# Performance work log

Measured on AMD Instinct MI355X. Metric: run time of the kernel, lower is better.

## Reference

```python
import jax, jax.numpy as jnp
import numpy as np

IN_DIM, MEM_DIM, NUM_WORDS, N_LEAVES = 300, 256, 50000, 8192


def setup_inputs() -> dict:
    key = jax.random.key(0)
    ks = jax.random.split(key, 6)
    s = 0.05
    return {
        "embs": jax.random.normal(ks[0], (N_LEAVES, IN_DIM), jnp.float32),
        "Wx": jax.random.normal(ks[1], (4 * MEM_DIM, IN_DIM), jnp.float32) * s,
        "bx": jax.random.normal(ks[2], (4 * MEM_DIM,), jnp.float32) * s,
        "Wl": jax.random.normal(ks[3], (5 * MEM_DIM, MEM_DIM), jnp.float32) * s,
        "Wr": jax.random.normal(ks[4], (5 * MEM_DIM, MEM_DIM), jnp.float32) * s,
        "emb_table": jax.random.normal(ks[5], (NUM_WORDS, IN_DIM), jnp.float32),
    }


def reference(embs, Wx, bx, Wl, Wr, emb_table):
    m = Wl.shape[1]

    # x-projection order along fused axis: [cx, ix, fx, ox]
    def proj_x(x):  # [B, in] -> [B, 4, m]
        return (x @ Wx.T + bx).reshape(x.shape[0], 4, m)

    # hidden-projection order: [u, i, lf, rf, o]
    def compose(xg, lc, lh, rc, rh):
        lg = (lh @ Wl.T).reshape(-1, 5, m)
        rg = (rh @ Wr.T).reshape(-1, 5, m)
        u = jnp.tanh(xg[:, 0] + lg[:, 0] + rg[:, 0])
        i = jax.nn.sigmoid(xg[:, 1] + lg[:, 1] + rg[:, 1])
        lf = jax.nn.sigmoid(xg[:, 2] + lg[:, 2] + rg[:, 2])  # fx shared
        rf = jax.nn.sigmoid(xg[:, 2] + lg[:, 3] + rg[:, 3])  # fx shared
        c = i * u + lf * lc + rf * rc
        o = jax.nn.sigmoid(xg[:, 3] + lg[:, 4] + rg[:, 4])
        h = o * jnp.tanh(c)
        return c, h

    # leaves: zero child states, per-leaf embedding inputs
    L = embs.shape[0]
    z = jnp.zeros((L, m), embs.dtype)
    c, h = compose(proj_x(embs), z, z, z, z)

    # internal nodes (PAD=True): input is word_embedding(num_words - 1)
    pad_xg = proj_x(emb_table[-1:])  # [1, 4, m]

    while c.shape[0] > 1:  # static shapes; 13 merge levels
        lc, rc = c[0::2], c[1::2]
        lh, rh = h[0::2], h[1::2]
        B = lc.shape[0]
        c, h = compose(jnp.broadcast_to(pad_xg, (B, 4, m)), lc, lh, rc, rh)

    return jnp.stack([c, h])  # root (c, h): [2, 1, mem_dim]
```

## Files before the change

### kernel.cpp

```cpp
#include <hip/hip_runtime.h>
#include <math.h>


#define MEM 256

typedef __attribute__((ext_vector_type(8))) short bf16x8;
typedef __attribute__((ext_vector_type(4))) float f32x4;

__device__ __forceinline__ float sigf(float x) { return 1.0f / (1.0f + __expf(-x)); }

__device__ __forceinline__ unsigned short f2b(float f) {
  unsigned int u = __float_as_uint(f);
  u = (u + 0x7FFFu + ((u >> 16) & 1u)) >> 16;
  return (unsigned short)u;
}

#define NB_WCF 2560
#define NB_WXF 960
#define NB_EB 10240
__global__ __launch_bounds__(256) void k_prep(
    const float* __restrict__ Wl, const float* __restrict__ Wr,
    const float* __restrict__ Wx, const float* __restrict__ bx,
    const float* __restrict__ embs, const float* __restrict__ emb_last,
    unsigned short* __restrict__ Wcf, unsigned short* __restrict__ Wxf,
    unsigned short* __restrict__ eb, float* __restrict__ bias5) {
  int b = blockIdx.x;
  if (b < NB_WCF) {
    int idx = b * 256 + threadIdx.x;
    int f = idx >> 9, r = idx & 511;
    int lane = r >> 3, j = r & 7;
    int gate = f % 5, t = f / 5;
    int grp = t & 15, kc = t >> 4;
    int k = kc * 32 + ((lane >> 4) << 3) + j;
    int n = gate * 256 + (grp << 4) + (lane & 15);
    float v = (k < 256) ? Wl[n * 256 + k] : Wr[n * 256 + (k - 256)];
    Wcf[idx] = f2b(v);
  } else if (b < NB_WCF + NB_WXF) {
    int idx = (b - NB_WCF) * 256 + threadIdx.x;
    int f = idx >> 9, r = idx & 511;
    int lane = r >> 3, j = r & 7;
    int gate = f % 3, t = f / 3;
    int grp = t & 15, kc = t >> 4;
    int k = kc * 32 + ((lane >> 4) << 3) + j;
    const int gmap[3] = {0, 1, 3};
    int n = gmap[gate] * 256 + (grp << 4) + (lane & 15);
    float v = (k < 300) ? Wx[n * 300 + k] : 0.0f;
    Wxf[idx] = f2b(v);
  } else if (b < NB_WCF + NB_WXF + NB_EB) {
    int idx = (b - NB_WCF - NB_WXF) * 256 + threadIdx.x;
    int row = idx / 320;
    int k = idx - row * 320;
    eb[idx] = (k < 300) ? f2b(embs[row * 300 + k]) : (unsigned short)0;
  } else {
    int g = b - (NB_WCF + NB_WXF + NB_EB);
    __shared__ float er[300];
    for (int k = threadIdx.x; k < 300; k += 256) er[k] = emb_last[k];
    __syncthreads();
    const int map[5] = {0, 1, 2, 2, 3};
    int wrow = map[g] * 256 + threadIdx.x;
    const float* w = Wx + wrow * 300;
    float s = bx[wrow];
    for (int k = 0; k < 300; k++) s += er[k] * w[k];
    bias5[g * 256 + threadIdx.x] = s;
  }
}

__global__ __launch_bounds__(256) void k_leaf_mfma(
    const unsigned short* __restrict__ eb, const unsigned short* __restrict__ Wxf,
    const float* __restrict__ bx, float* __restrict__ cO,
    unsigned short* __restrict__ hO) {
  int lane = threadIdx.x & 63;
  int wave = threadIdx.x >> 6;
  int grp = blockIdx.y;
  int tb = (blockIdx.x * 4 + wave) * 2;
  int m = lane & 15, quad = lane >> 4;

  f32x4 acc[2][3];
#pragma unroll
  for (int rt = 0; rt < 2; rt++)
#pragma unroll
    for (int g = 0; g < 3; g++) acc[rt][g] = (f32x4){0.f, 0.f, 0.f, 0.f};

  const unsigned short* ar0 = eb + (tb * 16 + m) * 320 + quad * 8;
  const unsigned short* ar1 = eb + ((tb + 1) * 16 + m) * 320 + quad * 8;
#pragma unroll
  for (int kc = 0; kc < 10; kc++) {
    const unsigned short* bp = Wxf + ((kc * 16 + grp) * 3) * 512 + lane * 8;
    bf16x8 b0 = *(const bf16x8*)(bp);
    bf16x8 b1 = *(const bf16x8*)(bp + 512);
    bf16x8 b2 = *(const bf16x8*)(bp + 1024);
    bf16x8 a0 = *(const bf16x8*)(ar0 + kc * 32);
    bf16x8 a1 = *(const bf16x8*)(ar1 + kc * 32);
    acc[0][0] = __builtin_amdgcn_mfma_f32_16x16x32_bf16(a0, b0, acc[0][0], 0, 0, 0);
    acc[0][1] = __builtin_amdgcn_mfma_f32_16x16x32_bf16(a0, b1, acc[0][1], 0, 0, 0);
    acc[0][2] = __builtin_amdgcn_mfma_f32_16x16x32_bf16(a0, b2, acc[0][2], 0, 0, 0);
    acc[1][0] = __builtin_amdgcn_mfma_f32_16x16x32_bf16(a1, b0, acc[1][0], 0, 0, 0);
    acc[1][1] = __builtin_amdgcn_mfma_f32_16x16x32_bf16(a1, b1, acc[1][1], 0, 0, 0);
    acc[1][2] = __builtin_amdgcn_mfma_f32_16x16x32_bf16(a1, b2, acc[1][2], 0, 0, 0);
  }
  int col = grp * 16 + m;
  float b0 = bx[col], b1 = bx[256 + col], b3 = bx[768 + col];
#pragma unroll
  for (int rt = 0; rt < 2; rt++) {
#pragma unroll
    for (int reg = 0; reg < 4; reg++) {
      int row = (tb + rt) * 16 + quad * 4 + reg;
      float u = tanhf(acc[rt][0][reg] + b0);
      float ig = sigf(acc[rt][1][reg] + b1);
      float o = sigf(acc[rt][2][reg] + b3);
      float c = ig * u;
      cO[row * MEM + col] = c;
      hO[row * MEM + col] = f2b(o * tanhf(c));
    }
  }
}

template <int RT>
__global__ __launch_bounds__(256) void k_compose_mfma(
    const unsigned short* __restrict__ hprev,
    const float* __restrict__ cprev,
    const unsigned short* __restrict__ Wcf, const float* __restrict__ bias5,
    float* __restrict__ cO, unsigned short* __restrict__ hO,
    float* __restrict__ hOf,
    int B) {
  int lane = threadIdx.x & 63;
  int wave = threadIdx.x >> 6;
  int grp = blockIdx.y;
  int tb = (blockIdx.x * 4 + wave) * RT;
  if (tb * 16 >= B) return;
  int m = lane & 15, quad = lane >> 4;
  const bf16x8 zz = {0, 0, 0, 0, 0, 0, 0, 0};

  f32x4 acc[RT][5];
  const unsigned short* ar[RT];
  bool ok[RT];
#pragma unroll
  for (int rt = 0; rt < RT; rt++) {
    int ra = (tb + rt) * 16 + m;
    ok[rt] = (ra < B);
    ar[rt] = hprev + ra * 512 + quad * 8;
#pragma unroll
    for (int g = 0; g < 5; g++) acc[rt][g] = (f32x4){0.f, 0.f, 0.f, 0.f};
  }

#pragma unroll
  for (int kc = 0; kc < 16; kc++) {
    const unsigned short* bp = Wcf + ((kc * 16 + grp) * 5) * 512 + lane * 8;
    bf16x8 b0 = *(const bf16x8*)(bp);
    bf16x8 b1 = *(const bf16x8*)(bp + 512);
    bf16x8 b2 = *(const bf16x8*)(bp + 1024);
    bf16x8 b3 = *(const bf16x8*)(bp + 1536);
    bf16x8 b4 = *(const bf16x8*)(bp + 2048);
#pragma unroll
    for (int rt = 0; rt < RT; rt++) {
      bf16x8 a = ok[rt] ? *(const bf16x8*)(ar[rt] + kc * 32) : zz;
      acc[rt][0] = __builtin_amdgcn_mfma_f32_16x16x32_bf16(a, b0, acc[rt][0], 0, 0, 0);
      acc[rt][1] = __builtin_amdgcn_mfma_f32_16x16x32_bf16(a, b1, acc[rt][1], 0, 0, 0);
      acc[rt][2] = __builtin_amdgcn_mfma_f32_16x16x32_bf16(a, b2, acc[rt][2], 0, 0, 0);
      acc[rt][3] = __builtin_amdgcn_mfma_f32_16x16x32_bf16(a, b3, acc[rt][3], 0, 0, 0);
      acc[rt][4] = __builtin_amdgcn_mfma_f32_16x16x32_bf16(a, b4, acc[rt][4], 0, 0, 0);
    }
  }
  int col = grp * 16 + m;
  float b0 = bias5[col], b1 = bias5[256 + col], b2 = bias5[512 + col];
  float b3 = bias5[768 + col], b4 = bias5[1024 + col];
#pragma unroll
  for (int rt = 0; rt < RT; rt++) {
#pragma unroll
    for (int reg = 0; reg < 4; reg++) {
      int row = (tb + rt) * 16 + quad * 4 + reg;
      if (row >= B) continue;
      float u = tanhf(acc[rt][0][reg] + b0);
      float ig = sigf(acc[rt][1][reg] + b1);
      float lf = sigf(acc[rt][2][reg] + b2);
      float rf = sigf(acc[rt][3][reg] + b3);
      float o = sigf(acc[rt][4][reg] + b4);
      float lc = cprev[(2 * row) * MEM + col];
      float rc = cprev[(2 * row + 1) * MEM + col];
      float c = ig * u + lf * lc + rf * rc;
      float h = o * tanhf(c);
      cO[row * MEM + col] = c;
      hO[row * MEM + col] = f2b(h);
      if (hOf) hOf[row * MEM + col] = h;
    }
  }
}

extern "C" void kernel_launch(void* const* d_in, const int* in_sizes, int n_in,
                              void* d_out, int out_size, void* d_ws, size_t ws_size,
                              hipStream_t stream) {
  const float* embs = (const float*)d_in[0];
  const float* Wx = (const float*)d_in[1];
  const float* bx = (const float*)d_in[2];
  const float* Wl = (const float*)d_in[3];
  const float* Wr = (const float*)d_in[4];
  const float* emb_table = (const float*)d_in[5];
  float* out = (float*)d_out;

  float* ws = (float*)d_ws;
  float* cA = ws;
  float* cB = cA + 8192 * 256;
  float* bias5 = cB + 4096 * 256;
  unsigned short* hA = (unsigned short*)(bias5 + 1280);
  unsigned short* hB = hA + 8192 * 256;
  unsigned short* Wcf = hB + 4096 * 256;
  unsigned short* Wxf = Wcf + 1280 * 512;
  unsigned short* eb = Wxf + 480 * 512;

  k_prep<<<NB_WCF + NB_WXF + NB_EB + 5, 256, 0, stream>>>(
      Wl, Wr, Wx, bx, embs, emb_table + (in_sizes[5] - 300),
      Wcf, Wxf, eb, bias5);

  k_leaf_mfma<<<dim3(64, 16), 256, 0, stream>>>(eb, Wxf, bx, cA, hA);

  const float* cs = cA;
  const unsigned short* hs = hA;
  int B = 4096;
  int lvl = 0;
  while (B >= 1) {
    float* dc;
    unsigned short* dh;
    float* dhf = nullptr;
    if (B == 1) {
      dc = out;
      dh = hB;
      dhf = out + 256;
    } else if ((lvl & 1) == 0) {
      dc = cB; dh = hB;
    } else {
      dc = cA; dh = hA;
    }
    int tiles = (B + 15) / 16;
    if (B == 4096) {
      k_compose_mfma<2><<<dim3(tiles / 8, 16), 256, 0, stream>>>(
          hs, cs, Wcf, bias5, dc, dh, dhf, B);
    } else {
      int gx = (tiles + 3) / 4;
      k_compose_mfma<1><<<dim3(gx, 16), 256, 0, stream>>>(
          hs, cs, Wcf, bias5, dc, dh, dhf, B);
    }
    cs = dc;
    hs = dh;
    B >>= 1;
    lvl++;
  }
}
```

Before: 260.9 us.

## Fuse leaf projection into prep kernel and add K-split compose for small levels

The leaf LSTM step now reads fp32 embeddings and Wx directly, converting them to bf16 on the fly inside the MFMA loop. The pre-converted eb/Wxf buffers and the separate leaf kernel launch are gone, and the leaf work runs in the same launch as the Wcf repack and bias computation. For tree levels with fewer than 64 nodes, a new kernel splits the K dimension across the four waves and reduces the partial sums through LDS, so small levels get more parallelism. The cost is that leaf blocks redundantly convert Wx per block and now do uncoalesced fp32 loads, and they also depend on no shared data with the prep blocks running alongside them.

After: 265.1 us. About the same (+1.6%).

```diff
diff --git a/kernel.cpp b/kernel.cpp
--- a/kernel.cpp
+++ b/kernel.cpp
@@ -1,4 +1,5 @@
 #include <hip/hip_runtime.h>
+#include <hip/hip_bf16.h>
 #include <math.h>
 
 
@@ -15,18 +16,88 @@
   return (unsigned short)u;
 }
 
+__device__ __forceinline__ unsigned short cvt1(float f) {
+  __hip_bfloat16 b = __float2bfloat16(f);
+  return *reinterpret_cast<unsigned short*>(&b);
+}
+
+__device__ __forceinline__ bf16x8 gather8(const float* __restrict__ rowp, int k0) {
+  bf16x8 r;
+  if (k0 + 8 <= 300) {
+    const float4 f0 = *(const float4*)(rowp + k0);
+    const float4 f1 = *(const float4*)(rowp + k0 + 4);
+    r[0] = cvt1(f0.x); r[1] = cvt1(f0.y); r[2] = cvt1(f0.z); r[3] = cvt1(f0.w);
+    r[4] = cvt1(f1.x); r[5] = cvt1(f1.y); r[6] = cvt1(f1.z); r[7] = cvt1(f1.w);
+  } else {
+#pragma unroll
+    for (int j = 0; j < 8; j++) {
+      int k = k0 + j;
+      r[j] = (k < 300) ? (short)cvt1(rowp[k]) : (short)0;
+    }
+  }
+  return r;
+}
+
+#define NB_LEAF 1024
 #define NB_WCF 2560
-#define NB_WXF 960
-#define NB_EB 10240
-__global__ __launch_bounds__(256) void k_prep(
-    const float* __restrict__ Wl, const float* __restrict__ Wr,
-    const float* __restrict__ Wx, const float* __restrict__ bx,
-    const float* __restrict__ embs, const float* __restrict__ emb_last,
-    unsigned short* __restrict__ Wcf, unsigned short* __restrict__ Wxf,
-    unsigned short* __restrict__ eb, float* __restrict__ bias5) {
+__global__ __launch_bounds__(256) void k_fused(
+    const float* __restrict__ embs, const float* __restrict__ Wx,
+    const float* __restrict__ bx, const float* __restrict__ Wl,
+    const float* __restrict__ Wr, const float* __restrict__ emb_last,
+    unsigned short* __restrict__ Wcf, float* __restrict__ bias5,
+    float* __restrict__ cO, unsigned short* __restrict__ hO) {
   int b = blockIdx.x;
-  if (b < NB_WCF) {
-    int idx = b * 256 + threadIdx.x;
+  int tid = threadIdx.x;
+  if (b < NB_LEAF) {
+    int grp = b & 15, rblk = b >> 4;
+    int lane = tid & 63, wave = tid >> 6;
+    int tb = (rblk * 4 + wave) * 2;
+    int m = lane & 15, quad = lane >> 4;
+    const int gmap[3] = {0, 1, 3};
+
+    f32x4 acc[2][3];
+#pragma unroll
+    for (int rt = 0; rt < 2; rt++)
+#pragma unroll
+      for (int g = 0; g < 3; g++) acc[rt][g] = (f32x4){0.f, 0.f, 0.f, 0.f};
+
+    const float* ar0 = embs + (tb * 16 + m) * 300;
+    const float* ar1 = embs + ((tb + 1) * 16 + m) * 300;
+    const float* wr0 = Wx + (gmap[0] * 256 + grp * 16 + m) * 300;
+    const float* wr1 = Wx + (gmap[1] * 256 + grp * 16 + m) * 300;
+    const float* wr2 = Wx + (gmap[2] * 256 + grp * 16 + m) * 300;
+#pragma unroll
+    for (int kc = 0; kc < 10; kc++) {
+      int k0 = kc * 32 + quad * 8;
+      bf16x8 a0 = gather8(ar0, k0);
+      bf16x8 a1 = gather8(ar1, k0);
+      bf16x8 w0 = gather8(wr0, k0);
+      acc[0][0] = __builtin_amdgcn_mfma_f32_16x16x32_bf16(a0, w0, acc[0][0], 0, 0, 0);
+      acc[1][0] = __builtin_amdgcn_mfma_f32_16x16x32_bf16(a1, w0, acc[1][0], 0, 0, 0);
+      bf16x8 w1 = gather8(wr1, k0);
+      acc[0][1] = __builtin_amdgcn_mfma_f32_16x16x32_bf16(a0, w1, acc[0][1], 0, 0, 0);
+      acc[1][1] = __builtin_amdgcn_mfma_f32_16x16x32_bf16(a1, w1, acc[1][1], 0, 0, 0);
+      bf16x8 w2 = gather8(wr2, k0);
+      acc[0][2] = __builtin_amdgcn_mfma_f32_16x16x32_bf16(a0, w2, acc[0][2], 0, 0, 0);
+      acc[1][2] = __builtin_amdgcn_mfma_f32_16x16x32_bf16(a1, w2, acc[1][2], 0, 0, 0);
+    }
+    int col = grp * 16 + m;
+    float b0 = bx[col], b1 = bx[256 + col], b3 = bx[768 + col];
+#pragma unroll
+    for (int rt = 0; rt < 2; rt++) {
+#pragma unroll
+      for (int reg = 0; reg < 4; reg++) {
+        int row = (tb + rt) * 16 + quad * 4 + reg;
+        float u = tanhf(acc[rt][0][reg] + b0);
+        float ig = sigf(acc[rt][1][reg] + b1);
+        float o = sigf(acc[rt][2][reg] + b3);
+        float c = ig * u;
+        cO[row * MEM + col] = c;
+        hO[row * MEM + col] = f2b(o * tanhf(c));
+      }
+    }
+  } else if (b < NB_LEAF + NB_WCF) {
+    int idx = (b - NB_LEAF) * 256 + tid;
     int f = idx >> 9, r = idx & 511;
     int lane = r >> 3, j = r & 7;
     int gate = f % 5, t = f / 5;
@@ -35,83 +106,17 @@
     int n = gate * 256 + (grp << 4) + (lane & 15);
     float v = (k < 256) ? Wl[n * 256 + k] : Wr[n * 256 + (k - 256)];
     Wcf[idx] = f2b(v);
-  } else if (b < NB_WCF + NB_WXF) {
-    int idx = (b - NB_WCF) * 256 + threadIdx.x;
-    int f = idx >> 9, r = idx & 511;
-    int lane = r >> 3, j = r & 7;
-    int gate = f % 3, t = f / 3;
-    int grp = t & 15, kc = t >> 4;
-    int k = kc * 32 + ((lane >> 4) << 3) + j;
-    const int gmap[3] = {0, 1, 3};
-    int n = gmap[gate] * 256 + (grp << 4) + (lane & 15);
-    float v = (k < 300) ? Wx[n * 300 + k] : 0.0f;
-    Wxf[idx] = f2b(v);
-  } else if (b < NB_WCF + NB_WXF + NB_EB) {
-    int idx = (b - NB_WCF - NB_WXF) * 256 + threadIdx.x;
-    int row = idx / 320;
-    int k = idx - row * 320;
-    eb[idx] = (k < 300) ? f2b(embs[row * 300 + k]) : (unsigned short)0;
   } else {
-    int g = b - (NB_WCF + NB_WXF + NB_EB);
+    int g = b - (NB_LEAF + NB_WCF);
     __shared__ float er[300];
-    for (int k = threadIdx.x; k < 300; k += 256) er[k] = emb_last[k];
+    for (int k = tid; k < 300; k += 256) er[k] = emb_last[k];
     __syncthreads();
     const int map[5] = {0, 1, 2, 2, 3};
-    int wrow = map[g] * 256 + threadIdx.x;
+    int wrow = map[g] * 256 + tid;
     const float* w = Wx + wrow * 300;
     float s = bx[wrow];
     for (int k = 0; k < 300; k++) s += er[k] * w[k];
-    bias5[g * 256 + threadIdx.x] = s;
-  }
-}
-
-__global__ __launch_bounds__(256) void k_leaf_mfma(
-    const unsigned short* __restrict__ eb, const unsigned short* __restrict__ Wxf,
-    const float* __restrict__ bx, float* __restrict__ cO,
-    unsigned short* __restrict__ hO) {
-  int lane = threadIdx.x & 63;
-  int wave = threadIdx.x >> 6;
-  int grp = blockIdx.y;
-  int tb = (blockIdx.x * 4 + wave) * 2;
-  int m = lane & 15, quad = lane >> 4;
-
-  f32x4 acc[2][3];
-#pragma unroll
-  for (int rt = 0; rt < 2; rt++)
-#pragma unroll
-    for (int g = 0; g < 3; g++) acc[rt][g] = (f32x4){0.f, 0.f, 0.f, 0.f};
-
-  const unsigned short* ar0 = eb + (tb * 16 + m) * 320 + quad * 8;
-  const unsigned short* ar1 = eb + ((tb + 1) * 16 + m) * 320 + quad * 8;
-#pragma unroll
-  for (int kc = 0; kc < 10; kc++) {
-    const unsigned short* bp = Wxf + ((kc * 16 + grp) * 3) * 512 + lane * 8;
-    bf16x8 b0 = *(const bf16x8*)(bp);
-    bf16x8 b1 = *(const bf16x8*)(bp + 512);
-    bf16x8 b2 = *(const bf16x8*)(bp + 1024);
-    bf16x8 a0 = *(const bf16x8*)(ar0 + kc * 32);
-    bf16x8 a1 = *(const bf16x8*)(ar1 + kc * 32);
-    acc[0][0] = __builtin_amdgcn_mfma_f32_16x16x32_bf16(a0, b0, acc[0][0], 0, 0, 0);
-    acc[0][1] = __builtin_amdgcn_mfma_f32_16x16x32_bf16(a0, b1, acc[0][1], 0, 0, 0);
-    acc[0][2] = __builtin_amdgcn_mfma_f32_16x16x32_bf16(a0, b2, acc[0][2], 0, 0, 0);
-    acc[1][0] = __builtin_amdgcn_mfma_f32_16x16x32_bf16(a1, b0, acc[1][0], 0, 0, 0);
-    acc[1][1] = __builtin_amdgcn_mfma_f32_16x16x32_bf16(a1, b1, acc[1][1], 0, 0, 0);
-    acc[1][2] = __builtin_amdgcn_mfma_f32_16x16x32_bf16(a1, b2, acc[1][2], 0, 0, 0);
-  }
-  int col = grp * 16 + m;
-  float b0 = bx[col], b1 = bx[256 + col], b3 = bx[768 + col];
-#pragma unroll
-  for (int rt = 0; rt < 2; rt++) {
-#pragma unroll
-    for (int reg = 0; reg < 4; reg++) {
-      int row = (tb + rt) * 16 + quad * 4 + reg;
-      float u = tanhf(acc[rt][0][reg] + b0);
-      float ig = sigf(acc[rt][1][reg] + b1);
-      float o = sigf(acc[rt][2][reg] + b3);
-      float c = ig * u;
-      cO[row * MEM + col] = c;
-      hO[row * MEM + col] = f2b(o * tanhf(c));
-    }
+    bias5[g * 256 + tid] = s;
   }
 }
 
@@ -121,8 +126,7 @@
     const float* __restrict__ cprev,
     const unsigned short* __restrict__ Wcf, const float* __restrict__ bias5,
     float* __restrict__ cO, unsigned short* __restrict__ hO,
-    float* __restrict__ hOf,
-    int B) {
+    float* __restrict__ hOf, int B) {
   int lane = threadIdx.x & 63;
   int wave = threadIdx.x >> 6;
   int grp = blockIdx.y;
@@ -186,6 +190,95 @@
   }
 }
 
+__global__ __launch_bounds__(256) void k_compose_ksplit(
+    const unsigned short* __restrict__ hprev, const float* __restrict__ cprev,
+    const unsigned short* __restrict__ Wcf, const float* __restrict__ bias5,
+    float* __restrict__ cO, unsigned short* __restrict__ hO,
+    float* __restrict__ hOf, int B) {
+  __shared__ __align__(16) float lds[4 * 2 * 5 * 64 * 4];
+  int tid = threadIdx.x;
+  int lane = tid & 63, wave = tid >> 6;
+  int grp = blockIdx.y;
+  int m = lane & 15, quad = lane >> 4;
+  int tiles = (B + 15) >> 4;
+  const bf16x8 zz = {0, 0, 0, 0, 0, 0, 0, 0};
+
+  f32x4 acc[2][5];
+  bool ok[2];
+  const unsigned short* ar[2];
+#pragma unroll
+  for (int t = 0; t < 2; t++) {
+    int ra = t * 16 + m;
+    ok[t] = (t < tiles) && (ra < B);
+    ar[t] = hprev + ra * 512 + quad * 8;
+#pragma unroll
+    for (int q = 0; q < 5; q++) acc[t][q] = (f32x4){0.f, 0.f, 0.f, 0.f};
+  }
+
+#pragma unroll
+  for (int kcl = 0; kcl < 4; kcl++) {
+    int kc = wave * 4 + kcl;
+    const unsigned short* bp = Wcf + ((kc * 16 + grp) * 5) * 512 + lane * 8;
+    bf16x8 b0 = *(const bf16x8*)(bp);
+    bf16x8 b1 = *(const bf16x8*)(bp + 512);
+    bf16x8 b2 = *(const bf16x8*)(bp + 1024);
+    bf16x8 b3 = *(const bf16x8*)(bp + 1536);
+    bf16x8 b4 = *(const bf16x8*)(bp + 2048);
+#pragma unroll
+    for (int t = 0; t < 2; t++) {
+      if (t < tiles) {
+        bf16x8 a = ok[t] ? *(const bf16x8*)(ar[t] + kc * 32) : zz;
+        acc[t][0] = __builtin_amdgcn_mfma_f32_16x16x32_bf16(a, b0, acc[t][0], 0, 0, 0);
+        acc[t][1] = __builtin_amdgcn_mfma_f32_16x16x32_bf16(a, b1, acc[t][1], 0, 0, 0);
+        acc[t][2] = __builtin_amdgcn_mfma_f32_16x16x32_bf16(a, b2, acc[t][2], 0, 0, 0);
+        acc[t][3] = __builtin_amdgcn_mfma_f32_16x16x32_bf16(a, b3, acc[t][3], 0, 0, 0);
+        acc[t][4] = __builtin_amdgcn_mfma_f32_16x16x32_bf16(a, b4, acc[t][4], 0, 0, 0);
+      }
+    }
+  }
+#pragma unroll
+  for (int t = 0; t < 2; t++)
+    if (t < tiles)
+#pragma unroll
+      for (int q = 0; q < 5; q++)
+        *(f32x4*)&lds[(((wave * 2 + t) * 5 + q) * 64 + lane) * 4] = acc[t][q];
+  __syncthreads();
+
+  if (wave < tiles) {
+    int t = wave;
+    int col = grp * 16 + m;
+    float b0 = bias5[col], b1 = bias5[256 + col], b2 = bias5[512 + col];
+    float b3 = bias5[768 + col], b4 = bias5[1024 + col];
+    f32x4 s[5];
+#pragma unroll
+    for (int q = 0; q < 5; q++) {
+      s[q] = *(const f32x4*)&lds[(((0 * 2 + t) * 5 + q) * 64 + lane) * 4];
+#pragma unroll
+      for (int v = 1; v < 4; v++) {
+        f32x4 p = *(const f32x4*)&lds[(((v * 2 + t) * 5 + q) * 64 + lane) * 4];
+        s[q][0] += p[0]; s[q][1] += p[1]; s[q][2] += p[2]; s[q][3] += p[3];
+      }
+    }
+#pragma unroll
+    for (int reg = 0; reg < 4; reg++) {
+      int row = t * 16 + quad * 4 + reg;
+      if (row >= B) continue;
+      float u = tanhf(s[0][reg] + b0);
+      float ig = sigf(s[1][reg] + b1);
+      float lf = sigf(s[2][reg] + b2);
+      float rf = sigf(s[3][reg] + b3);
+      float o = sigf(s[4][reg] + b4);
+      float lc = cprev[(2 * row) * MEM + col];
+      float rc = cprev[(2 * row + 1) * MEM + col];
+      float c = ig * u + lf * lc + rf * rc;
+      float h = o * tanhf(c);
+      cO[row * MEM + col] = c;
+      hO[row * MEM + col] = f2b(h);
+      if (hOf) hOf[row * MEM + col] = h;
+    }
+  }
+}
+
 extern "C" void kernel_launch(void* const* d_in, const int* in_sizes, int n_in,
                               void* d_out, int out_size, void* d_ws, size_t ws_size,
                               hipStream_t stream) {
@@ -204,14 +297,10 @@
   unsigned short* hA = (unsigned short*)(bias5 + 1280);
   unsigned short* hB = hA + 8192 * 256;
   unsigned short* Wcf = hB + 4096 * 256;
-  unsigned short* Wxf = Wcf + 1280 * 512;
-  unsigned short* eb = Wxf + 480 * 512;
-
-  k_prep<<<NB_WCF + NB_WXF + NB_EB + 5, 256, 0, stream>>>(
-      Wl, Wr, Wx, bx, embs, emb_table + (in_sizes[5] - 300),
-      Wcf, Wxf, eb, bias5);
-
-  k_leaf_mfma<<<dim3(64, 16), 256, 0, stream>>>(eb, Wxf, bx, cA, hA);
+
+  k_fused<<<NB_LEAF + NB_WCF + 5, 256, 0, stream>>>(
+      embs, Wx, bx, Wl, Wr, emb_table + (in_sizes[5] - 300),
+      Wcf, bias5, cA, hA);
 
   const float* cs = cA;
   const unsigned short* hs = hA;
@@ -234,9 +323,12 @@
     if (B == 4096) {
       k_compose_mfma<2><<<dim3(tiles / 8, 16), 256, 0, stream>>>(
           hs, cs, Wcf, bias5, dc, dh, dhf, B);
-    } else {
+    } else if (B >= 64) {
       int gx = (tiles + 3) / 4;
       k_compose_mfma<1><<<dim3(gx, 16), 256, 0, stream>>>(
+          hs, cs, Wcf, bias5, dc, dh, dhf, B);
+    } else {
+      k_compose_ksplit<<<dim3(1, 16), 256, 0, stream>>>(
           hs, cs, Wcf, bias5, dc, dh, dhf, B);
     }
     cs = dc;
```
